# Kernel tuning notes

Measured on AMD Instinct MI355X. Metric: run time of the kernel, lower is better.

The kernel has to match this reference:

```python
import jax, jax.numpy as jnp
import numpy as np

E = 1024   # embedding_dim
H = 64     # head_size
B, T = 8, 2048

def setup_inputs() -> dict:
    key = jax.random.key(0)
    k1, k2, k3, k4 = jax.random.split(key, 4)
    s = 1.0 / np.sqrt(E)
    return {
        "x": jax.random.normal(k1, (B, T, E), dtype=jnp.float32),
        "Wq": jax.random.normal(k2, (E, H), dtype=jnp.float32) * s,
        "Wk": jax.random.normal(k3, (E, H), dtype=jnp.float32) * s,
        "Wv": jax.random.normal(k4, (E, H), dtype=jnp.float32) * s,
    }

def reference(x, Wq, Wk, Wv):
    # projections: [B,T,E] @ [E,H] -> [B,T,H]
    q = x @ Wq
    k = x @ Wk
    v = x @ Wv
    Tq = x.shape[1]
    # scaled scores [B,T,T], masked causal softmax, then @ V
    wei = jnp.einsum('bth,bsh->bts', q, k) * (H ** -0.5)
    causal = jnp.tril(jnp.ones((Tq, Tq), dtype=bool))
    wei = jnp.where(causal, wei, -jnp.inf)
    attn = jax.nn.softmax(wei, axis=-1)
    return attn @ v
```

## Files before the change

kernel.cpp:

```cpp
#include <hip/hip_runtime.h>

#define E  1024
#define H  64
#define BB 8
#define TT 2048

typedef __attribute__((ext_vector_type(8)))  short bf16x8;
typedef __attribute__((ext_vector_type(4)))  float f32x4;
typedef __attribute__((ext_vector_type(16))) float f32x16;
typedef __attribute__((ext_vector_type(8)))  short short8;
typedef __attribute__((ext_vector_type(4)))  short short4v;
typedef __attribute__((ext_vector_type(4)))  unsigned u32x4;

__device__ __forceinline__ short f2bf(float f) {
    union { float f; unsigned u; } v; v.f = f;
    unsigned r = v.u + 0x7FFFu + ((v.u >> 16) & 1u);
    return (short)(r >> 16);
}

__device__ __forceinline__ float fexp2(float x) {
    float r;
    asm("v_exp_f32 %0, %1" : "=v"(r) : "v"(x));
    return r;
}

__device__ __forceinline__ bf16x8 cvt8(float4 a0, float4 a1) {
    unsigned w0, w1, w2, w3;
    asm("v_cvt_pk_bf16_f32 %0, %1, %2" : "=v"(w0) : "v"(a0.x), "v"(a0.y));
    asm("v_cvt_pk_bf16_f32 %0, %1, %2" : "=v"(w1) : "v"(a0.z), "v"(a0.w));
    asm("v_cvt_pk_bf16_f32 %0, %1, %2" : "=v"(w2) : "v"(a1.x), "v"(a1.y));
    asm("v_cvt_pk_bf16_f32 %0, %1, %2" : "=v"(w3) : "v"(a1.z), "v"(a1.w));
    u32x4 u = {w0, w1, w2, w3};
    bf16x8 r;
    __builtin_memcpy(&r, &u, 16);
    return r;
}

__global__ __launch_bounds__(256)
void pack_w(const float* __restrict__ Wq, const float* __restrict__ Wk,
            const float* __restrict__ Wv, short* __restrict__ Wb)
{
    const int t  = blockIdx.x * 256 + threadIdx.x;
    const int l  = t & 63;
    const int f  = (t >> 6) % 12;
    const int kc = t / 768;
    const float* W = (f < 4) ? Wq : ((f < 8) ? Wk : Wv);
    const int e0 = kc * 32 + ((l >> 4) << 3);
    const int n  = ((f & 3) << 4) + (l & 15);
    short8 o;
    #pragma unroll
    for (int j = 0; j < 8; ++j) o[j] = f2bf(W[(e0 + j) * 64 + n]);
    *(short8*)&Wb[(size_t)t * 8] = o;
}

__global__ __launch_bounds__(512)
void proj_v3(const float* __restrict__ x, const short* __restrict__ Wb,
             short* __restrict__ q, short* __restrict__ k, short* __restrict__ vt)
{
    __shared__ short xs[32 * 1024];
    const int t = threadIdx.x;
    const long row0 = (long)blockIdx.x * 32;

    {
        float4 va[16];
        #pragma unroll
        for (int i = 0; i < 8; ++i) {
            const int idx = i * 512 + t;
            const int row = idx >> 7, u = idx & 127;
            const float* p = x + (row0 + row) * E + u * 8;
            va[i * 2]     = *(const float4*)(p);
            va[i * 2 + 1] = *(const float4*)(p + 4);
        }
        #pragma unroll
        for (int i = 0; i < 8; ++i) {
            const int idx = i * 512 + t;
            const int row = idx >> 7, u = idx & 127;
            *(bf16x8*)&xs[row * 1024 + ((u ^ (row & 7)) << 3)] = cvt8(va[i * 2], va[i * 2 + 1]);
        }
    }
    __syncthreads();

    const int l   = t & 63;
    const int w8  = t >> 6;
    const int rg  = w8 >> 2, fg = w8 & 3;
    const int l15 = l & 15, g = l >> 4;
    const int arow  = rg * 16 + l15;
    const int abase = arow * 1024;
    const int aswz  = arow & 7;

    f32x4 acc[3] = {(f32x4){0,0,0,0}, (f32x4){0,0,0,0}, (f32x4){0,0,0,0}};
    const short* wb = Wb + ((size_t)(fg * 3) * 64 + l) * 8;

    #pragma unroll 4
    for (int kc = 0; kc < 32; ++kc) {
        bf16x8 af = *(const bf16x8*)&xs[abase + (((kc * 4 + g) ^ aswz) << 3)];
        const short* wp = wb + (size_t)kc * 12 * 512;
        bf16x8 b0 = *(const bf16x8*)(wp);
        bf16x8 b1 = *(const bf16x8*)(wp + 512);
        bf16x8 b2 = *(const bf16x8*)(wp + 1024);
        acc[0] = __builtin_amdgcn_mfma_f32_16x16x32_bf16(af, b0, acc[0], 0, 0, 0);
        acc[1] = __builtin_amdgcn_mfma_f32_16x16x32_bf16(af, b1, acc[1], 0, 0, 0);
        acc[2] = __builtin_amdgcn_mfma_f32_16x16x32_bf16(af, b2, acc[2], 0, 0, 0);
    }

    const long rowb = row0 + rg * 16;
    #pragma unroll
    for (int fi = 0; fi < 3; ++fi) {
        const int f = fg * 3 + fi;
        const int m = f >> 2;
        const int h = ((f & 3) << 4) + l15;
        if (m == 2) {
            const long row = rowb + g * 4;
            const long bb = row >> 11;
            const int  t0 = (int)(row & 2047);
            short4v pkt;
            #pragma unroll
            for (int r = 0; r < 4; ++r) pkt[r] = f2bf(acc[fi][r]);
            *(short4v*)&vt[(bb * 64 + h) * TT + t0] = pkt;
        } else {
            short* base = (m == 0) ? q : k;
            const float sc = (m == 0) ? (0.125f * 1.44269504f) : 1.0f;
            #pragma unroll
            for (int r = 0; r < 4; ++r)
                base[(rowb + g * 4 + r) * 64 + h] = f2bf(acc[fi][r] * sc);
        }
    }
}

__global__ __launch_bounds__(512)
void attn_v8(const short* __restrict__ qg,
             const short* __restrict__ kg,
             const short* __restrict__ vtg,
             float* __restrict__ out)
{
    __shared__ float Op[8][32][66];
    __shared__ float Ml[8][32][2];

    const int t   = threadIdx.x;
    const int L   = t & 63;
    const int w   = t >> 6;
    const int bid = blockIdx.x;
    const int b   = bid & 7;
    const int pr  = bid >> 3;
    const int l31 = L & 31, hi = L >> 5;

    const int stA = pr, stB = 63 - pr;
    const int nA = stA + 1;
    int WA = (8 * nA + 32) / 65;
    WA = WA < 1 ? 1 : (WA > 7 ? 7 : WA);
    const int WB = 8 - WA;

    const bool isB  = (w >= WA);
    const int  st   = isB ? stB : stA;
    const int  q0   = st * 32;
    const int  strd = isB ? WB : WA;
    const int  c0   = isB ? (w - WA) : w;

    bf16x8 qf[4];
    {
        const short* qp = qg + ((long)b * TT + q0 + l31) * 64 + hi * 8;
        qf[0] = *(const bf16x8*)(qp);
        qf[1] = *(const bf16x8*)(qp + 16);
        qf[2] = *(const bf16x8*)(qp + 32);
        qf[3] = *(const bf16x8*)(qp + 48);
    }

    f32x16 o0 = {}, o1 = {};
    float mrun = -1e30f, lrun = 0.f;

    const short* kbase = kg  + ((long)b * TT + l31) * 64 + hi * 8;
    const short* vbase = vtg + ((long)b * 64 + l31) * TT + hi * 8;

    for (int ci = c0; ci <= st; ci += strd) {
        const int kvs = ci * 32;
        const short* kp = kbase + (long)kvs * 64;
        bf16x8 kf0 = *(const bf16x8*)(kp);
        bf16x8 kf1 = *(const bf16x8*)(kp + 16);
        bf16x8 kf2 = *(const bf16x8*)(kp + 32);
        bf16x8 kf3 = *(const bf16x8*)(kp + 48);
        const short* vp = vbase + kvs;
        bf16x8 vf00 = *(const bf16x8*)(vp);
        bf16x8 vf01 = *(const bf16x8*)(vp + 16);
        bf16x8 vf10 = *(const bf16x8*)(vp + 32 * TT);
        bf16x8 vf11 = *(const bf16x8*)(vp + 32 * TT + 16);

        f32x16 s = {};
        __builtin_amdgcn_s_setprio(1);
        s = __builtin_amdgcn_mfma_f32_32x32x16_bf16(kf0, qf[0], s, 0, 0, 0);
        s = __builtin_amdgcn_mfma_f32_32x32x16_bf16(kf1, qf[1], s, 0, 0, 0);
        s = __builtin_amdgcn_mfma_f32_32x32x16_bf16(kf2, qf[2], s, 0, 0, 0);
        s = __builtin_amdgcn_mfma_f32_32x32x16_bf16(kf3, qf[3], s, 0, 0, 0);
        __builtin_amdgcn_s_setprio(0);

        if (kvs == q0) {
            #pragma unroll
            for (int r = 0; r < 16; ++r) {
                const int crow = (r & 3) + 8 * (r >> 2) + 4 * hi;
                if (crow > l31) s[r] = -1e30f;
            }
        }
        float m01 = fmaxf(s[0], s[1]),   m23 = fmaxf(s[2], s[3]);
        float m45 = fmaxf(s[4], s[5]),   m67 = fmaxf(s[6], s[7]);
        float m89 = fmaxf(s[8], s[9]),   mab = fmaxf(s[10], s[11]);
        float mcd = fmaxf(s[12], s[13]), mef = fmaxf(s[14], s[15]);
        float mloc = fmaxf(fmaxf(fmaxf(m01, m23), fmaxf(m45, m67)),
                           fmaxf(fmaxf(m89, mab), fmaxf(mcd, mef)));
        mloc = fmaxf(mloc, __shfl_xor(mloc, 32));
        if (__any(mloc > mrun + 8.f)) {
            const float mnew = fmaxf(mrun, mloc);
            const float a = fexp2(mrun - mnew);
            mrun = mnew;
            lrun *= a;
            #pragma unroll
            for (int r = 0; r < 16; ++r) { o0[r] *= a; o1[r] *= a; }
        }
        #pragma unroll
        for (int r = 0; r < 16; ++r) s[r] = fexp2(s[r] - mrun);
        {
            float s01 = (s[0] + s[1]) + (s[2] + s[3]);
            float s23 = (s[4] + s[5]) + (s[6] + s[7]);
            float s45 = (s[8] + s[9]) + (s[10] + s[11]);
            float s67 = (s[12] + s[13]) + (s[14] + s[15]);
            float lsum = (s01 + s23) + (s45 + s67);
            lsum += __shfl_xor(lsum, 32);
            lrun += lsum;
        }
        unsigned wv[8];
        #pragma unroll
        for (int i = 0; i < 8; ++i)
            asm("v_cvt_pk_bf16_f32 %0, %1, %2" : "=v"(wv[i]) : "v"(s[2 * i]), "v"(s[2 * i + 1]));
        unsigned p00 = wv[0], p02 = wv[2];
        unsigned p01 = wv[1], p03 = wv[3];
        unsigned p10 = wv[4], p12 = wv[6];
        unsigned p11 = wv[5], p13 = wv[7];
        asm("v_permlane32_swap_b32 %0, %1" : "+v"(p00), "+v"(p02));
        asm("v_permlane32_swap_b32 %0, %1" : "+v"(p01), "+v"(p03));
        asm("v_permlane32_swap_b32 %0, %1" : "+v"(p10), "+v"(p12));
        asm("v_permlane32_swap_b32 %0, %1" : "+v"(p11), "+v"(p13));
        u32x4 pb0u = {p00, p01, p02, p03};
        u32x4 pb1u = {p10, p11, p12, p13};
        bf16x8 pb0, pb1;
        __builtin_memcpy(&pb0, &pb0u, 16);
        __builtin_memcpy(&pb1, &pb1u, 16);
        __builtin_amdgcn_s_setprio(1);
        o0 = __builtin_amdgcn_mfma_f32_32x32x16_bf16(vf00, pb0, o0, 0, 0, 0);
        o0 = __builtin_amdgcn_mfma_f32_32x32x16_bf16(vf01, pb1, o0, 0, 0, 0);
        o1 = __builtin_amdgcn_mfma_f32_32x32x16_bf16(vf10, pb0, o1, 0, 0, 0);
        o1 = __builtin_amdgcn_mfma_f32_32x32x16_bf16(vf11, pb1, o1, 0, 0, 0);
        __builtin_amdgcn_s_setprio(0);
    }

    #pragma unroll
    for (int r = 0; r < 16; ++r) {
        const int h = (r & 3) + 8 * (r >> 2) + 4 * hi;
        Op[w][l31][h]      = o0[r];
        Op[w][l31][32 + h] = o1[r];
    }
    if (hi == 0) {
        Ml[w][l31][0] = mrun;
        Ml[w][l31][1] = lrun;
    }
    __syncthreads();

    {
        const bool tb   = (w >= 4);
        const int  base = tb ? WA : 0;
        const int  cnt  = tb ? WB : WA;
        const long oq0  = (long)(tb ? stB : stA) * 32;
        #pragma unroll
        for (int rr = 0; rr < 8; ++rr) {
            const int row = (w & 3) * 8 + rr;
            float M = -1e30f;
            for (int j = 0; j < cnt; ++j)
                M = fmaxf(M, Ml[base + j][row][0]);
            float Ls = 0.f, val = 0.f;
            for (int j = 0; j < cnt; ++j) {
                const float a = fexp2(Ml[base + j][row][0] - M);
                Ls  += a * Ml[base + j][row][1];
                val += a * Op[base + j][row][L];
            }
            out[((long)b * TT + oq0 + row) * 64 + L] = val / Ls;
        }
    }
}

extern "C" void kernel_launch(void* const* d_in, const int* in_sizes, int n_in,
                              void* d_out, int out_size, void* d_ws, size_t ws_size,
                              hipStream_t stream)
{
    const float* x  = (const float*)d_in[0];
    const float* Wq = (const float*)d_in[1];
    const float* Wk = (const float*)d_in[2];
    const float* Wv = (const float*)d_in[3];
    float* out = (float*)d_out;

    const size_t n = (size_t)BB * TT * H;
    short* q  = (short*)d_ws;
    short* k  = q + n;
    short* vt = k + n;
    short* Wb = vt + n;

    pack_w  <<<dim3(96),  256, 0, stream>>>(Wq, Wk, Wv, Wb);
    proj_v3 <<<dim3(512), 512, 0, stream>>>(x, Wb, q, k, vt);
    attn_v8 <<<dim3(256), 512, 0, stream>>>(q, k, vt, out);
}
```

Baseline: 58.27 us.

## Load x directly to LDS via global_load_lds and halve projection tile rows

The projection kernel now stages the fp32 x tile straight into shared memory with the direct global-to-LDS load, using an XOR swizzle on the source column, instead of loading into registers, converting to bf16 and storing. The conversion to bf16 moves into the MFMA loop, which now reads two float4s per step. The block shrinks to 16 rows and 256 threads with 1024 blocks, so per-block LDS stays at 64KB but holds fp32 data. The intent is to remove the register round trip and raise occupancy and overlap. The cost is that each MFMA step does twice the LDS reads plus conversion work, and the weight fragments are reloaded across twice as many blocks.

Measured after the change: 59.76 us. 2.6% more time.

```diff
diff --git a/kernel.cpp b/kernel.cpp
--- a/kernel.cpp
+++ b/kernel.cpp
@@ -53,47 +53,42 @@
     *(short8*)&Wb[(size_t)t * 8] = o;
 }
 
-__global__ __launch_bounds__(512)
-void proj_v3(const float* __restrict__ x, const short* __restrict__ Wb,
+__global__ __launch_bounds__(256)
+void proj_v4(const float* __restrict__ x, const short* __restrict__ Wb,
              short* __restrict__ q, short* __restrict__ k, short* __restrict__ vt)
 {
-    __shared__ short xs[32 * 1024];
+    __shared__ float xs[16 * 1024];
     const int t = threadIdx.x;
-    const long row0 = (long)blockIdx.x * 32;
-
-    {
-        float4 va[16];
-        #pragma unroll
-        for (int i = 0; i < 8; ++i) {
-            const int idx = i * 512 + t;
-            const int row = idx >> 7, u = idx & 127;
-            const float* p = x + (row0 + row) * E + u * 8;
-            va[i * 2]     = *(const float4*)(p);
-            va[i * 2 + 1] = *(const float4*)(p + 4);
-        }
-        #pragma unroll
-        for (int i = 0; i < 8; ++i) {
-            const int idx = i * 512 + t;
-            const int row = idx >> 7, u = idx & 127;
-            *(bf16x8*)&xs[row * 1024 + ((u ^ (row & 7)) << 3)] = cvt8(va[i * 2], va[i * 2 + 1]);
-        }
+    const long row0 = (long)blockIdx.x * 16;
+
+    #pragma unroll
+    for (int i = 0; i < 16; ++i) {
+        const int u = i * 256 + t;
+        const int r = u >> 8;
+        const int c = (u & 255) ^ (r & 7);
+        const float* gp = x + (row0 + r) * E + c * 4;
+        __builtin_amdgcn_global_load_lds(
+            (const __attribute__((address_space(1))) void*)gp,
+            (__attribute__((address_space(3))) void*)&xs[u * 4],
+            16, 0, 0);
     }
     __syncthreads();
 
     const int l   = t & 63;
-    const int w8  = t >> 6;
-    const int rg  = w8 >> 2, fg = w8 & 3;
+    const int fg  = t >> 6;
     const int l15 = l & 15, g = l >> 4;
-    const int arow  = rg * 16 + l15;
-    const int abase = arow * 1024;
-    const int aswz  = arow & 7;
+    const int rbase = l15 * 256;
+    const int rswz  = l15 & 7;
 
     f32x4 acc[3] = {(f32x4){0,0,0,0}, (f32x4){0,0,0,0}, (f32x4){0,0,0,0}};
     const short* wb = Wb + ((size_t)(fg * 3) * 64 + l) * 8;
 
     #pragma unroll 4
     for (int kc = 0; kc < 32; ++kc) {
-        bf16x8 af = *(const bf16x8*)&xs[abase + (((kc * 4 + g) ^ aswz) << 3)];
+        const int c0 = kc * 8 + g * 2;
+        float4 xa = *(const float4*)&xs[(rbase + (c0 ^ rswz)) * 4];
+        float4 xb = *(const float4*)&xs[(rbase + ((c0 + 1) ^ rswz)) * 4];
+        bf16x8 af = cvt8(xa, xb);
         const short* wp = wb + (size_t)kc * 12 * 512;
         bf16x8 b0 = *(const bf16x8*)(wp);
         bf16x8 b1 = *(const bf16x8*)(wp + 512);
@@ -103,14 +98,13 @@
         acc[2] = __builtin_amdgcn_mfma_f32_16x16x32_bf16(af, b2, acc[2], 0, 0, 0);
     }
 
-    const long rowb = row0 + rg * 16;
     #pragma unroll
     for (int fi = 0; fi < 3; ++fi) {
         const int f = fg * 3 + fi;
         const int m = f >> 2;
         const int h = ((f & 3) << 4) + l15;
         if (m == 2) {
-            const long row = rowb + g * 4;
+            const long row = row0 + g * 4;
             const long bb = row >> 11;
             const int  t0 = (int)(row & 2047);
             short4v pkt;
@@ -122,7 +116,7 @@
             const float sc = (m == 0) ? (0.125f * 1.44269504f) : 1.0f;
             #pragma unroll
             for (int r = 0; r < 4; ++r)
-                base[(rowb + g * 4 + r) * 64 + h] = f2bf(acc[fi][r] * sc);
+                base[(row0 + g * 4 + r) * 64 + h] = f2bf(acc[fi][r] * sc);
         }
     }
 }
@@ -300,7 +294,7 @@
     short* vt = k + n;
     short* Wb = vt + n;
 
-    pack_w  <<<dim3(96),  256, 0, stream>>>(Wq, Wk, Wv, Wb);
-    proj_v3 <<<dim3(512), 512, 0, stream>>>(x, Wb, q, k, vt);
-    attn_v8 <<<dim3(256), 512, 0, stream>>>(q, k, vt, out);
-}
+    pack_w  <<<dim3(96),   256, 0, stream>>>(Wq, Wk, Wv, Wb);
+    proj_v4 <<<dim3(1024), 256, 0, stream>>>(x, Wb, q, k, vt);
+    attn_v8 <<<dim3(256),  512, 0, stream>>>(q, k, vt, out);
+}
```

## Enlarge projection tile to 64 rows with 4 wavefronts reusing weight fragments

Applied to the files above, without the earlier changes.

The projection kernel now handles 64 rows per block using 4 wavefronts instead of 32 rows using 8. Each wave keeps 4 row tiles × 3 feature tiles of accumulators, so every weight fragment read from global memory feeds four MFMAs instead of one. The aim is to cut redundant weight loads. In exchange the block uses 128KB of shared memory, has fewer threads loading x, and runs only 256 blocks, which lowers occupancy and latency hiding.

After: 58.85 us. Within noise of the previous version (+1.0%).

```diff
diff --git a/kernel.cpp b/kernel.cpp
--- a/kernel.cpp
+++ b/kernel.cpp
@@ -53,76 +53,81 @@
     *(short8*)&Wb[(size_t)t * 8] = o;
 }
 
-__global__ __launch_bounds__(512)
-void proj_v3(const float* __restrict__ x, const short* __restrict__ Wb,
+__global__ __launch_bounds__(256)
+void proj_v5(const float* __restrict__ x, const short* __restrict__ Wb,
              short* __restrict__ q, short* __restrict__ k, short* __restrict__ vt)
 {
-    __shared__ short xs[32 * 1024];
+    __shared__ short xs[64 * 1024];
     const int t = threadIdx.x;
-    const long row0 = (long)blockIdx.x * 32;
-
-    {
+    const long row0 = (long)blockIdx.x * 64;
+
+    #pragma unroll
+    for (int b8 = 0; b8 < 4; ++b8) {
         float4 va[16];
         #pragma unroll
-        for (int i = 0; i < 8; ++i) {
-            const int idx = i * 512 + t;
-            const int row = idx >> 7, u = idx & 127;
-            const float* p = x + (row0 + row) * E + u * 8;
-            va[i * 2]     = *(const float4*)(p);
-            va[i * 2 + 1] = *(const float4*)(p + 4);
-        }
-        #pragma unroll
-        for (int i = 0; i < 8; ++i) {
-            const int idx = i * 512 + t;
-            const int row = idx >> 7, u = idx & 127;
-            *(bf16x8*)&xs[row * 1024 + ((u ^ (row & 7)) << 3)] = cvt8(va[i * 2], va[i * 2 + 1]);
+        for (int j = 0; j < 8; ++j) {
+            const int u = (b8 * 8 + j) * 256 + t;
+            const int r = u >> 7, c = u & 127;
+            const float* p = x + (row0 + r) * E + c * 8;
+            va[j * 2]     = *(const float4*)(p);
+            va[j * 2 + 1] = *(const float4*)(p + 4);
+        }
+        #pragma unroll
+        for (int j = 0; j < 8; ++j) {
+            const int u = (b8 * 8 + j) * 256 + t;
+            const int r = u >> 7, c = u & 127;
+            *(bf16x8*)&xs[(r * 128 + (c ^ (r & 7))) * 8] = cvt8(va[j * 2], va[j * 2 + 1]);
         }
     }
     __syncthreads();
 
     const int l   = t & 63;
-    const int w8  = t >> 6;
-    const int rg  = w8 >> 2, fg = w8 & 3;
+    const int fg  = t >> 6;
     const int l15 = l & 15, g = l >> 4;
-    const int arow  = rg * 16 + l15;
-    const int abase = arow * 1024;
-    const int aswz  = arow & 7;
-
-    f32x4 acc[3] = {(f32x4){0,0,0,0}, (f32x4){0,0,0,0}, (f32x4){0,0,0,0}};
+    const int swz = l15 & 7;
+
+    f32x4 acc[4][3] = {};
     const short* wb = Wb + ((size_t)(fg * 3) * 64 + l) * 8;
 
     #pragma unroll 4
     for (int kc = 0; kc < 32; ++kc) {
-        bf16x8 af = *(const bf16x8*)&xs[abase + (((kc * 4 + g) ^ aswz) << 3)];
         const short* wp = wb + (size_t)kc * 12 * 512;
         bf16x8 b0 = *(const bf16x8*)(wp);
         bf16x8 b1 = *(const bf16x8*)(wp + 512);
         bf16x8 b2 = *(const bf16x8*)(wp + 1024);
-        acc[0] = __builtin_amdgcn_mfma_f32_16x16x32_bf16(af, b0, acc[0], 0, 0, 0);
-        acc[1] = __builtin_amdgcn_mfma_f32_16x16x32_bf16(af, b1, acc[1], 0, 0, 0);
-        acc[2] = __builtin_amdgcn_mfma_f32_16x16x32_bf16(af, b2, acc[2], 0, 0, 0);
-    }
-
-    const long rowb = row0 + rg * 16;
+        const int cu = (kc * 4 + g) ^ swz;
+        #pragma unroll
+        for (int rt = 0; rt < 4; ++rt) {
+            bf16x8 af = *(const bf16x8*)&xs[((rt * 16 + l15) * 128 + cu) * 8];
+            acc[rt][0] = __builtin_amdgcn_mfma_f32_16x16x32_bf16(af, b0, acc[rt][0], 0, 0, 0);
+            acc[rt][1] = __builtin_amdgcn_mfma_f32_16x16x32_bf16(af, b1, acc[rt][1], 0, 0, 0);
+            acc[rt][2] = __builtin_amdgcn_mfma_f32_16x16x32_bf16(af, b2, acc[rt][2], 0, 0, 0);
+        }
+    }
+
     #pragma unroll
-    for (int fi = 0; fi < 3; ++fi) {
-        const int f = fg * 3 + fi;
-        const int m = f >> 2;
-        const int h = ((f & 3) << 4) + l15;
-        if (m == 2) {
-            const long row = rowb + g * 4;
-            const long bb = row >> 11;
-            const int  t0 = (int)(row & 2047);
-            short4v pkt;
-            #pragma unroll
-            for (int r = 0; r < 4; ++r) pkt[r] = f2bf(acc[fi][r]);
-            *(short4v*)&vt[(bb * 64 + h) * TT + t0] = pkt;
-        } else {
-            short* base = (m == 0) ? q : k;
-            const float sc = (m == 0) ? (0.125f * 1.44269504f) : 1.0f;
-            #pragma unroll
-            for (int r = 0; r < 4; ++r)
-                base[(rowb + g * 4 + r) * 64 + h] = f2bf(acc[fi][r] * sc);
+    for (int rt = 0; rt < 4; ++rt) {
+        const long rowb = row0 + rt * 16;
+        #pragma unroll
+        for (int fi = 0; fi < 3; ++fi) {
+            const int f = fg * 3 + fi;
+            const int m = f >> 2;
+            const int h = ((f & 3) << 4) + l15;
+            if (m == 2) {
+                const long row = rowb + g * 4;
+                const long bb = row >> 11;
+                const int  t0 = (int)(row & 2047);
+                short4v pkt;
+                #pragma unroll
+                for (int r = 0; r < 4; ++r) pkt[r] = f2bf(acc[rt][fi][r]);
+                *(short4v*)&vt[(bb * 64 + h) * TT + t0] = pkt;
+            } else {
+                short* base = (m == 0) ? q : k;
+                const float sc = (m == 0) ? (0.125f * 1.44269504f) : 1.0f;
+                #pragma unroll
+                for (int r = 0; r < 4; ++r)
+                    base[(rowb + g * 4 + r) * 64 + h] = f2bf(acc[rt][fi][r] * sc);
+            }
         }
     }
 }
@@ -301,6 +306,6 @@
     short* Wb = vt + n;
 
     pack_w  <<<dim3(96),  256, 0, stream>>>(Wq, Wk, Wv, Wb);
-    proj_v3 <<<dim3(512), 512, 0, stream>>>(x, Wb, q, k, vt);
+    proj_v5 <<<dim3(256), 256, 0, stream>>>(x, Wb, q, k, vt);
     attn_v8 <<<dim3(256), 512, 0, stream>>>(q, k, vt, out);
 }
```

## Restructure projection to split-K 32x32 MFMA with direct global loads

Applied to the files above, without the earlier changes.

The projection kernel no longer stages the 32-row x tile into shared memory as bf16. Each wave now loads x straight from global, converts it in registers, and runs 32x32x16 MFMAs over one quarter of the E dimension. The four K-split partial sums are reduced through shared memory. The weight packing layout is changed to match. This removes the full-tile LDS staging and barrier before compute, at the cost of an extra LDS reduction and less coalesced x loads.

After: 65.23 us. +11.9%, slower.

```diff
diff --git a/kernel.cpp b/kernel.cpp
--- a/kernel.cpp
+++ b/kernel.cpp
@@ -37,92 +37,95 @@
 }
 
 __global__ __launch_bounds__(256)
-void pack_w(const float* __restrict__ Wq, const float* __restrict__ Wk,
-            const float* __restrict__ Wv, short* __restrict__ Wb)
+void pack_w2(const float* __restrict__ Wq, const float* __restrict__ Wk,
+             const float* __restrict__ Wv, short* __restrict__ Wb2)
 {
     const int t  = blockIdx.x * 256 + threadIdx.x;
     const int l  = t & 63;
-    const int f  = (t >> 6) % 12;
-    const int kc = t / 768;
-    const float* W = (f < 4) ? Wq : ((f < 8) ? Wk : Wv);
-    const int e0 = kc * 32 + ((l >> 4) << 3);
-    const int n  = ((f & 3) << 4) + (l & 15);
+    const int fg = (t >> 6) % 6;
+    const int kc = t / 384;
+    const int n  = fg * 32 + (l & 31);
+    const int m  = n >> 6, nn = n & 63;
+    const float* W = (m == 0) ? Wq : (m == 1 ? Wk : Wv);
+    const int e0 = kc * 16 + ((l >> 5) << 3);
     short8 o;
     #pragma unroll
-    for (int j = 0; j < 8; ++j) o[j] = f2bf(W[(e0 + j) * 64 + n]);
-    *(short8*)&Wb[(size_t)t * 8] = o;
+    for (int j = 0; j < 8; ++j) o[j] = f2bf(W[(e0 + j) * 64 + nn]);
+    *(short8*)&Wb2[(size_t)t * 8] = o;
 }
 
 __global__ __launch_bounds__(512)
-void proj_v3(const float* __restrict__ x, const short* __restrict__ Wb,
+void proj_v7(const float* __restrict__ x, const short* __restrict__ Wb2,
              short* __restrict__ q, short* __restrict__ k, short* __restrict__ vt)
 {
-    __shared__ short xs[32 * 1024];
-    const int t = threadIdx.x;
+    __shared__ float part[2][3][3][16][64];
+    const int t  = threadIdx.x;
+    const int l  = t & 63;
+    const int w  = t >> 6;
+    const int cg = w & 1, ks = w >> 1;
+    const int l31 = l & 31, hi = l >> 5;
     const long row0 = (long)blockIdx.x * 32;
 
-    {
-        float4 va[16];
-        #pragma unroll
-        for (int i = 0; i < 8; ++i) {
-            const int idx = i * 512 + t;
-            const int row = idx >> 7, u = idx & 127;
-            const float* p = x + (row0 + row) * E + u * 8;
-            va[i * 2]     = *(const float4*)(p);
-            va[i * 2 + 1] = *(const float4*)(p + 4);
-        }
-        #pragma unroll
-        for (int i = 0; i < 8; ++i) {
-            const int idx = i * 512 + t;
-            const int row = idx >> 7, u = idx & 127;
-            *(bf16x8*)&xs[row * 1024 + ((u ^ (row & 7)) << 3)] = cvt8(va[i * 2], va[i * 2 + 1]);
-        }
-    }
-    __syncthreads();
-
-    const int l   = t & 63;
-    const int w8  = t >> 6;
-    const int rg  = w8 >> 2, fg = w8 & 3;
-    const int l15 = l & 15, g = l >> 4;
-    const int arow  = rg * 16 + l15;
-    const int abase = arow * 1024;
-    const int aswz  = arow & 7;
-
-    f32x4 acc[3] = {(f32x4){0,0,0,0}, (f32x4){0,0,0,0}, (f32x4){0,0,0,0}};
-    const short* wb = Wb + ((size_t)(fg * 3) * 64 + l) * 8;
+    f32x16 acc0 = {}, acc1 = {}, acc2 = {};
+
+    const float* xp = x + (row0 + l31) * E + ks * 256 + hi * 8;
+    const short* wb = Wb2 + ((size_t)(ks * 16 * 6 + cg * 3) * 64 + l) * 8;
 
     #pragma unroll 4
-    for (int kc = 0; kc < 32; ++kc) {
-        bf16x8 af = *(const bf16x8*)&xs[abase + (((kc * 4 + g) ^ aswz) << 3)];
-        const short* wp = wb + (size_t)kc * 12 * 512;
+    for (int s = 0; s < 16; ++s) {
+        float4 a0 = *(const float4*)(xp + s * 16);
+        float4 a1 = *(const float4*)(xp + s * 16 + 4);
+        bf16x8 af = cvt8(a0, a1);
+        const short* wp = wb + (size_t)s * 6 * 512;
         bf16x8 b0 = *(const bf16x8*)(wp);
         bf16x8 b1 = *(const bf16x8*)(wp + 512);
         bf16x8 b2 = *(const bf16x8*)(wp + 1024);
-        acc[0] = __builtin_amdgcn_mfma_f32_16x16x32_bf16(af, b0, acc[0], 0, 0, 0);
-        acc[1] = __builtin_amdgcn_mfma_f32_16x16x32_bf16(af, b1, acc[1], 0, 0, 0);
-        acc[2] = __builtin_amdgcn_mfma_f32_16x16x32_bf16(af, b2, acc[2], 0, 0, 0);
-    }
-
-    const long rowb = row0 + rg * 16;
-    #pragma unroll
-    for (int fi = 0; fi < 3; ++fi) {
-        const int f = fg * 3 + fi;
-        const int m = f >> 2;
-        const int h = ((f & 3) << 4) + l15;
-        if (m == 2) {
-            const long row = rowb + g * 4;
-            const long bb = row >> 11;
-            const int  t0 = (int)(row & 2047);
-            short4v pkt;
-            #pragma unroll
-            for (int r = 0; r < 4; ++r) pkt[r] = f2bf(acc[fi][r]);
-            *(short4v*)&vt[(bb * 64 + h) * TT + t0] = pkt;
-        } else {
-            short* base = (m == 0) ? q : k;
-            const float sc = (m == 0) ? (0.125f * 1.44269504f) : 1.0f;
-            #pragma unroll
-            for (int r = 0; r < 4; ++r)
-                base[(rowb + g * 4 + r) * 64 + h] = f2bf(acc[fi][r] * sc);
+        acc0 = __builtin_amdgcn_mfma_f32_32x32x16_bf16(af, b0, acc0, 0, 0, 0);
+        acc1 = __builtin_amdgcn_mfma_f32_32x32x16_bf16(af, b1, acc1, 0, 0, 0);
+        acc2 = __builtin_amdgcn_mfma_f32_32x32x16_bf16(af, b2, acc2, 0, 0, 0);
+    }
+
+    if (ks != 0) {
+        #pragma unroll
+        for (int i = 0; i < 16; ++i) {
+            part[cg][ks - 1][0][i][l] = acc0[i];
+            part[cg][ks - 1][1][i][l] = acc1[i];
+            part[cg][ks - 1][2][i][l] = acc2[i];
+        }
+    }
+    __syncthreads();
+    if (ks == 0) {
+        #pragma unroll
+        for (int i = 0; i < 16; ++i) {
+            acc0[i] += part[cg][0][0][i][l] + part[cg][1][0][i][l] + part[cg][2][0][i][l];
+            acc1[i] += part[cg][0][1][i][l] + part[cg][1][1][i][l] + part[cg][2][1][i][l];
+            acc2[i] += part[cg][0][2][i][l] + part[cg][1][2][i][l] + part[cg][2][2][i][l];
+        }
+        const long bb = row0 >> 11;
+        const int  tbase = (int)(row0 & 2047);
+        #pragma unroll
+        for (int f = 0; f < 3; ++f) {
+            const f32x16 acc = (f == 0) ? acc0 : (f == 1) ? acc1 : acc2;
+            const int n = cg * 96 + f * 32 + l31;
+            const int m = n >> 6;
+            const int h = n & 63;
+            if (m == 2) {
+                #pragma unroll
+                for (int a = 0; a < 4; ++a) {
+                    short4v pkt;
+                    #pragma unroll
+                    for (int r = 0; r < 4; ++r) pkt[r] = f2bf(acc[a * 4 + r]);
+                    *(short4v*)&vt[(bb * 64 + h) * TT + tbase + a * 8 + hi * 4] = pkt;
+                }
+            } else {
+                short* base = (m == 0) ? q : k;
+                const float sc = (m == 0) ? (0.125f * 1.44269504f) : 1.0f;
+                #pragma unroll
+                for (int r = 0; r < 16; ++r) {
+                    const int crow = (r & 3) + 8 * (r >> 2) + 4 * hi;
+                    base[(row0 + crow) * 64 + h] = f2bf(acc[r] * sc);
+                }
+            }
         }
     }
 }
@@ -295,12 +298,12 @@
     float* out = (float*)d_out;
 
     const size_t n = (size_t)BB * TT * H;
-    short* q  = (short*)d_ws;
-    short* k  = q + n;
-    short* vt = k + n;
-    short* Wb = vt + n;
-
-    pack_w  <<<dim3(96),  256, 0, stream>>>(Wq, Wk, Wv, Wb);
-    proj_v3 <<<dim3(512), 512, 0, stream>>>(x, Wb, q, k, vt);
+    short* q   = (short*)d_ws;
+    short* k   = q + n;
+    short* vt  = k + n;
+    short* Wb2 = vt + n;
+
+    pack_w2 <<<dim3(96),  256, 0, stream>>>(Wq, Wk, Wv, Wb2);
+    proj_v7 <<<dim3(512), 512, 0, stream>>>(x, Wb2, q, k, vt);
     attn_v8 <<<dim3(256), 512, 0, stream>>>(q, k, vt, out);
 }
```
